# Kernel tuning notes

Hardware: AMD Instinct MI355X
Metric: run time of the kernel (lower is better)

## Reference

```python
import jax, jax.numpy as jnp
import numpy as np

INPUT_DIM = 1024
HIDDEN_DIM = 1024

def setup_inputs() -> dict:
    key = jax.random.key(0)
    ks = jax.random.split(key, 9)
    s_in = 1.0 / np.sqrt(INPUT_DIM)
    s_h = 1.0 / np.sqrt(HIDDEN_DIM)
    x = jax.random.normal(ks[0], (4, 2048, INPUT_DIM), dtype=jnp.float32)
    Wq = jax.random.uniform(ks[1], (INPUT_DIM, HIDDEN_DIM), jnp.float32, -s_in, s_in)
    bq = jax.random.uniform(ks[2], (HIDDEN_DIM,), jnp.float32, -s_in, s_in)
    Wk = jax.random.uniform(ks[3], (INPUT_DIM, HIDDEN_DIM), jnp.float32, -s_in, s_in)
    bk = jax.random.uniform(ks[4], (HIDDEN_DIM,), jnp.float32, -s_in, s_in)
    Wv = jax.random.uniform(ks[5], (INPUT_DIM, HIDDEN_DIM), jnp.float32, -s_in, s_in)
    bv = jax.random.uniform(ks[6], (HIDDEN_DIM,), jnp.float32, -s_in, s_in)
    Wo = jax.random.uniform(ks[7], (HIDDEN_DIM, INPUT_DIM), jnp.float32, -s_h, s_h)
    bo = jax.random.uniform(ks[8], (INPUT_DIM,), jnp.float32, -s_h, s_h)
    return {"x": x, "Wq": Wq, "bq": bq, "Wk": Wk, "bk": bk, "Wv": Wv, "bv": bv, "Wo": Wo, "bo": bo}

def reference(x, Wq, bq, Wk, bk, Wv, bv, Wo, bo):
    # x: [B, S, D_in]; scale uses x.shape[-1] (faithful to source, which divides by sqrt(input_dim))
    scale = 1.0 / jnp.sqrt(jnp.asarray(x.shape[-1], dtype=x.dtype))
    Q = jnp.einsum('bsd,dh->bsh', x, Wq) + bq
    K = jnp.einsum('bsd,dh->bsh', x, Wk) + bk
    V = jnp.einsum('bsd,dh->bsh', x, Wv) + bv
    scores = jnp.einsum('bqh,bkh->bqk', Q, K) * scale  # [B, S, S]
    attn = jax.nn.softmax(scores, axis=-1)
    ctx = jnp.einsum('bqk,bkh->bqh', attn, V)
    return jnp.einsum('bsh,hd->bsd', ctx, Wo) + bo
```

## Files before the change

### kernel.cpp

```cpp
#include <hip/hip_runtime.h>
#include <hip/hip_bf16.h>

typedef __attribute__((ext_vector_type(8))) short bf16x8;
typedef __attribute__((ext_vector_type(16))) float f32x16;

#define AS1 __attribute__((address_space(1)))
#define AS3 __attribute__((address_space(3)))

__device__ __forceinline__ unsigned short f2bf(float f) {
  unsigned u = __float_as_uint(f);
  u += 0x7fff + ((u >> 16) & 1);
  return (unsigned short)(u >> 16);
}

__device__ __forceinline__ void gload_lds16(const void* g, void* l) {
  __builtin_amdgcn_global_load_lds((const AS1 unsigned int*)g,
                                   (AS3 unsigned int*)l, 16, 0, 0);
}

template <typename OutT, bool BIAS, bool SPLIT>
__global__ __launch_bounds__(256) void gemm_bt(
    const unsigned short* __restrict__ A,
    const unsigned short* __restrict__ Bt,
    OutT* __restrict__ C,
    const float* __restrict__ bias,
    int Kd, int lda, int ldb, int ldc,
    long sA, long sB, long sC,
    float scale) {
  __shared__ unsigned short ldsA[128 * 32];
  __shared__ unsigned short ldsB[128 * 32];
  const int bz = blockIdx.z;
  A  += (size_t)bz * sA + (size_t)blockIdx.x * 128 * lda;
  Bt += (size_t)bz * sB + (size_t)blockIdx.y * 128 * ldb;

  const int tid  = threadIdx.x;
  const int wave = tid >> 6;
  const int lane = tid & 63;
  const int wm   = (wave >> 1) * 64;
  const int wn   = (wave & 1) * 64;
  const int l32  = lane & 31;
  const int half = lane >> 5;
  const int srow = wave * 16 + (lane >> 2);
  const int cg   = ((lane & 3) ^ ((lane >> 2) & 3) ^ (lane >> 4)) * 8;
  const int pswz = (l32 & 3) ^ ((l32 >> 2) & 3);

  f32x16 acc[2][2] = {};

  for (int k0 = 0; k0 < Kd; k0 += 32) {
    __syncthreads();
    gload_lds16(A  + (size_t)srow * lda + k0 + cg,        (char*)ldsA + wave * 1024);
    gload_lds16(A  + (size_t)(srow + 64) * lda + k0 + cg, (char*)ldsA + 4096 + wave * 1024);
    gload_lds16(Bt + (size_t)srow * ldb + k0 + cg,        (char*)ldsB + wave * 1024);
    gload_lds16(Bt + (size_t)(srow + 64) * ldb + k0 + cg, (char*)ldsB + 4096 + wave * 1024);
    __syncthreads();

    bf16x8 af[2][2], bfr[2][2];
#pragma unroll
    for (int t = 0; t < 2; ++t)
#pragma unroll
      for (int h = 0; h < 2; ++h) {
        const int p = ((2 * h + half) ^ pswz) * 8;
        af[t][h]  = *(const bf16x8*)&ldsA[(wm + t * 32 + l32) * 32 + p];
        bfr[t][h] = *(const bf16x8*)&ldsB[(wn + t * 32 + l32) * 32 + p];
      }
#pragma unroll
    for (int t = 0; t < 2; ++t)
#pragma unroll
      for (int u = 0; u < 2; ++u) {
        acc[t][u] = __builtin_amdgcn_mfma_f32_32x32x16_bf16(af[t][0], bfr[u][0], acc[t][u], 0, 0, 0);
        acc[t][u] = __builtin_amdgcn_mfma_f32_32x32x16_bf16(af[t][1], bfr[u][1], acc[t][u], 0, 0, 0);
      }
  }

  const int row0 = blockIdx.x * 128 + wm;
  const int col0glob = blockIdx.y * 128 + wn;
  int col0;
  if constexpr (SPLIT) {
    C += (size_t)((blockIdx.y * 128) >> 10) * sC;
    col0 = ((blockIdx.y * 128) & 1023) + wn;
  } else {
    C += (size_t)bz * sC;
    col0 = col0glob;
  }
#pragma unroll
  for (int t = 0; t < 2; ++t) {
#pragma unroll
    for (int u = 0; u < 2; ++u) {
      const int col = col0 + u * 32 + l32;
      const float bv = BIAS ? bias[col0glob + u * 32 + l32] : 0.0f;
#pragma unroll
      for (int r = 0; r < 16; ++r) {
        const int row = row0 + t * 32 + (r & 3) + 8 * (r >> 2) + 4 * half;
        const float v = acc[t][u][r] * scale + bv;
        if constexpr (sizeof(OutT) == 4)
          C[(size_t)row * ldc + col] = v;
        else
          C[(size_t)row * ldc + col] = (OutT)f2bf(v);
      }
    }
  }
}

__global__ void cvt_x(const float* __restrict__ in, unsigned short* __restrict__ out, int n4) {
  const int i = blockIdx.x * blockDim.x + threadIdx.x;
  if (i < n4) {
    const float4 v = ((const float4*)in)[i];
    uint2 o;
    o.x = (unsigned)f2bf(v.x) | ((unsigned)f2bf(v.y) << 16);
    o.y = (unsigned)f2bf(v.z) | ((unsigned)f2bf(v.w) << 16);
    ((uint2*)out)[i] = o;
  }
}

__global__ void cvtT_w4(const float* __restrict__ Wq, const float* __restrict__ Wk,
                        const float* __restrict__ Wv, const float* __restrict__ Wo,
                        unsigned short* __restrict__ Wqkvb, unsigned short* __restrict__ Wob) {
  __shared__ unsigned short tile[64][65];
  const int z = blockIdx.z;
  const float* in = (z == 0) ? Wq : (z == 1) ? Wk : (z == 2) ? Wv : Wo;
  unsigned short* out = (z == 3) ? Wob : Wqkvb + (size_t)z * 1024 * 1024;
  const int r0 = blockIdx.y * 64, c0 = blockIdx.x * 64;
  for (int i = threadIdx.y; i < 64; i += 4)
    tile[i][threadIdx.x] = f2bf(in[(size_t)(r0 + i) * 1024 + c0 + threadIdx.x]);
  __syncthreads();
  for (int i = threadIdx.y; i < 64; i += 4)
    out[(size_t)(c0 + i) * 1024 + r0 + threadIdx.x] = tile[threadIdx.x][i];
}

__global__ void concat_bias(const float* __restrict__ bq, const float* __restrict__ bk,
                            const float* __restrict__ bv, float* __restrict__ dst) {
  const int z = blockIdx.x;
  const float* src = (z == 0) ? bq : (z == 1) ? bk : bv;
  const int i = threadIdx.x;
  ((float4*)(dst + z * 1024))[i] = ((const float4*)src)[i];
}

__global__ void transpose_bf16(const unsigned short* __restrict__ in,
                               unsigned short* __restrict__ out, int rows, int cols) {
  __shared__ unsigned short tile[64][65];
  const int b = blockIdx.z;
  in  += (size_t)b * rows * cols;
  out += (size_t)b * rows * cols;
  const int r0 = blockIdx.y * 64, c0 = blockIdx.x * 64;
  for (int i = threadIdx.y; i < 64; i += 4)
    tile[i][threadIdx.x] = in[(size_t)(r0 + i) * cols + c0 + threadIdx.x];
  __syncthreads();
  for (int i = threadIdx.y; i < 64; i += 4)
    out[(size_t)(c0 + i) * rows + r0 + threadIdx.x] = tile[threadIdx.x][i];
}

__global__ __launch_bounds__(256) void softmax_inplace(float* __restrict__ scores) {
  float* p = scores + (size_t)blockIdx.x * 2048;
  const int t = threadIdx.x;
  float4 v0 = ((const float4*)p)[t * 2];
  float4 v1 = ((const float4*)p)[t * 2 + 1];

  float m = fmaxf(fmaxf(fmaxf(v0.x, v0.y), fmaxf(v0.z, v0.w)),
                  fmaxf(fmaxf(v1.x, v1.y), fmaxf(v1.z, v1.w)));
#pragma unroll
  for (int off = 32; off; off >>= 1) m = fmaxf(m, __shfl_xor(m, off, 64));

  __shared__ float red[4];
  __shared__ float bcast[2];
  const int wave = t >> 6, lane = t & 63;
  if (lane == 0) red[wave] = m;
  __syncthreads();
  if (t == 0) bcast[0] = fmaxf(fmaxf(red[0], red[1]), fmaxf(red[2], red[3]));
  __syncthreads();
  m = bcast[0];

  v0.x = __expf(v0.x - m); v0.y = __expf(v0.y - m);
  v0.z = __expf(v0.z - m); v0.w = __expf(v0.w - m);
  v1.x = __expf(v1.x - m); v1.y = __expf(v1.y - m);
  v1.z = __expf(v1.z - m); v1.w = __expf(v1.w - m);

  float s = v0.x + v0.y + v0.z + v0.w + v1.x + v1.y + v1.z + v1.w;
#pragma unroll
  for (int off = 32; off; off >>= 1) s += __shfl_xor(s, off, 64);
  if (lane == 0) red[wave] = s;
  __syncthreads();
  if (t == 0) bcast[1] = red[0] + red[1] + red[2] + red[3];
  __syncthreads();
  const float inv = 1.0f / bcast[1];

  uint4 ov;
  ov.x = (unsigned)f2bf(v0.x * inv) | ((unsigned)f2bf(v0.y * inv) << 16);
  ov.y = (unsigned)f2bf(v0.z * inv) | ((unsigned)f2bf(v0.w * inv) << 16);
  ov.z = (unsigned)f2bf(v1.x * inv) | ((unsigned)f2bf(v1.y * inv) << 16);
  ov.w = (unsigned)f2bf(v1.z * inv) | ((unsigned)f2bf(v1.w * inv) << 16);
  ((uint4*)p)[t] = ov;
}

extern "C" void kernel_launch(void* const* d_in, const int* in_sizes, int n_in,
                              void* d_out, int out_size, void* d_ws, size_t ws_size,
                              hipStream_t stream) {
  const float* x  = (const float*)d_in[0];
  const float* Wq = (const float*)d_in[1];
  const float* bq = (const float*)d_in[2];
  const float* Wk = (const float*)d_in[3];
  const float* bk = (const float*)d_in[4];
  const float* Wv = (const float*)d_in[5];
  const float* bv = (const float*)d_in[6];
  const float* Wo = (const float*)d_in[7];
  const float* bo = (const float*)d_in[8];
  float* out = (float*)d_out;

  char* ws = (char*)d_ws;
  size_t off = 0;
  auto alloc = [&](size_t bytes) { char* p = ws + off; off += (bytes + 255) & ~255UL; return p; };
  unsigned short* xb    = (unsigned short*)alloc(8192UL * 1024 * 2);
  unsigned short* Wqkvb = (unsigned short*)alloc(3072UL * 1024 * 2);
  unsigned short* Wob   = (unsigned short*)alloc(1024UL * 1024 * 2);
  float*          bqkv  = (float*)alloc(3072UL * 4);
  unsigned short* Qb    = (unsigned short*)alloc(8192UL * 1024 * 2);
  unsigned short* Kb    = (unsigned short*)alloc(8192UL * 1024 * 2);
  unsigned short* Vb    = (unsigned short*)alloc(8192UL * 1024 * 2);
  unsigned short* Vtb   = (unsigned short*)alloc(4UL * 1024 * 2048 * 2);
  unsigned short* ctxb  = (unsigned short*)alloc(8192UL * 1024 * 2);
  float*          sc    = (float*)alloc(4UL * 2048 * 2048 * 4);

  const dim3 blk(256);

  cvt_x<<<2097152 / 256, 256, 0, stream>>>(x, xb, 2097152);
  cvtT_w4<<<dim3(16, 16, 4), dim3(64, 4), 0, stream>>>(Wq, Wk, Wv, Wo, Wqkvb, Wob);
  concat_bias<<<3, 256, 0, stream>>>(bq, bk, bv, bqkv);

  gemm_bt<unsigned short, true, true><<<dim3(64, 24, 1), blk, 0, stream>>>(
      xb, Wqkvb, Qb, bqkv, 1024, 1024, 1024, 1024, 0, 0, 8192L * 1024, 1.0f);

  transpose_bf16<<<dim3(16, 32, 4), dim3(64, 4), 0, stream>>>(Vb, Vtb, 2048, 1024);

  gemm_bt<float, false, false><<<dim3(16, 16, 4), blk, 0, stream>>>(
      Qb, Kb, sc, nullptr, 1024, 1024, 1024, 2048,
      2048L * 1024, 2048L * 1024, 2048L * 2048, 0.03125f);

  softmax_inplace<<<8192, 256, 0, stream>>>(sc);

  gemm_bt<unsigned short, false, false><<<dim3(16, 8, 4), blk, 0, stream>>>(
      (unsigned short*)sc, Vtb, ctxb, nullptr, 2048, 4096, 2048, 1024,
      2048L * 4096, 1024L * 2048, 2048L * 1024, 1.0f);

  gemm_bt<float, true, false><<<dim3(64, 8, 1), blk, 0, stream>>>(
      ctxb, Wob, out, bo, 1024, 1024, 1024, 1024, 0, 0, 0, 1.0f);
}
```

Baseline: 328.5 us.

## Double-buffer GEMM LDS staging and widen N tile for large GEMMs

The bf16 MFMA GEMM now issues global-to-LDS loads for the next K slice into a second LDS buffer before computing on the current one, dropping one barrier per iteration. A template parameter NJ also widens the block's N tile to 256 for the QKV projection and QK^T GEMMs, so each A tile is reused across more columns, with launch grids halved to match. Launch bounds are tightened to hint occupancy. In exchange, more LDS and accumulator registers are used per block, which may lower occupancy. With only one barrier per iteration, correctness depends on the asynchronous global_load_lds writes into the other buffer not racing with reads from the previous iteration.

```diff
diff --git a/kernel.cpp b/kernel.cpp
--- a/kernel.cpp
+++ b/kernel.cpp
@@ -18,8 +18,8 @@
                                    (AS3 unsigned int*)l, 16, 0, 0);
 }
 
-template <typename OutT, bool BIAS, bool SPLIT>
-__global__ __launch_bounds__(256) void gemm_bt(
+template <typename OutT, bool BIAS, bool SPLIT, int NJ>
+__global__ __launch_bounds__(256, (NJ == 4) ? 2 : 3) void gemm_bt(
     const unsigned short* __restrict__ A,
     const unsigned short* __restrict__ Bt,
     OutT* __restrict__ C,
@@ -27,67 +27,86 @@
     int Kd, int lda, int ldb, int ldc,
     long sA, long sB, long sC,
     float scale) {
-  __shared__ unsigned short ldsA[128 * 32];
-  __shared__ unsigned short ldsB[128 * 32];
+  constexpr int BN    = NJ * 64;
+  constexpr int ROWS  = 128 + BN;
+  constexpr int SLOTS = ROWS / 16;
+  __shared__ unsigned short lds[2][ROWS * 32];
+
   const int bz = blockIdx.z;
   A  += (size_t)bz * sA + (size_t)blockIdx.x * 128 * lda;
-  Bt += (size_t)bz * sB + (size_t)blockIdx.y * 128 * ldb;
+  Bt += (size_t)bz * sB + (size_t)blockIdx.y * BN * ldb;
 
   const int tid  = threadIdx.x;
   const int wave = tid >> 6;
   const int lane = tid & 63;
   const int wm   = (wave >> 1) * 64;
-  const int wn   = (wave & 1) * 64;
+  const int wn   = (wave & 1) * (NJ * 32);
   const int l32  = lane & 31;
   const int half = lane >> 5;
-  const int srow = wave * 16 + (lane >> 2);
   const int cg   = ((lane & 3) ^ ((lane >> 2) & 3) ^ (lane >> 4)) * 8;
   const int pswz = (l32 & 3) ^ ((l32 >> 2) & 3);
 
-  f32x16 acc[2][2] = {};
-
+  auto stage = [&](int k0, int b) {
+#pragma unroll
+    for (int j = 0; j < SLOTS / 4; ++j) {
+      const int s = wave + 4 * j;
+      const int r = s * 16 + (lane >> 2);
+      const unsigned short* src = (s < 8) ? (A + (size_t)r * lda)
+                                          : (Bt + (size_t)(r - 128) * ldb);
+      gload_lds16(src + k0 + cg, (char*)&lds[b][0] + s * 1024);
+    }
+  };
+
+  f32x16 acc[2][NJ] = {};
+
+  stage(0, 0);
+  int cur = 0;
   for (int k0 = 0; k0 < Kd; k0 += 32) {
     __syncthreads();
-    gload_lds16(A  + (size_t)srow * lda + k0 + cg,        (char*)ldsA + wave * 1024);
-    gload_lds16(A  + (size_t)(srow + 64) * lda + k0 + cg, (char*)ldsA + 4096 + wave * 1024);
-    gload_lds16(Bt + (size_t)srow * ldb + k0 + cg,        (char*)ldsB + wave * 1024);
-    gload_lds16(Bt + (size_t)(srow + 64) * ldb + k0 + cg, (char*)ldsB + 4096 + wave * 1024);
-    __syncthreads();
-
-    bf16x8 af[2][2], bfr[2][2];
+    if (k0 + 32 < Kd) stage(k0 + 32, cur ^ 1);
+
+    const unsigned short* base = &lds[cur][0];
+    bf16x8 af[2][2], bfr[NJ][2];
 #pragma unroll
     for (int t = 0; t < 2; ++t)
 #pragma unroll
       for (int h = 0; h < 2; ++h) {
         const int p = ((2 * h + half) ^ pswz) * 8;
-        af[t][h]  = *(const bf16x8*)&ldsA[(wm + t * 32 + l32) * 32 + p];
-        bfr[t][h] = *(const bf16x8*)&ldsB[(wn + t * 32 + l32) * 32 + p];
+        af[t][h] = *(const bf16x8*)&base[(wm + t * 32 + l32) * 32 + p];
+      }
+#pragma unroll
+    for (int u = 0; u < NJ; ++u)
+#pragma unroll
+      for (int h = 0; h < 2; ++h) {
+        const int p = ((2 * h + half) ^ pswz) * 8;
+        bfr[u][h] = *(const bf16x8*)&base[(128 + wn + u * 32 + l32) * 32 + p];
       }
 #pragma unroll
     for (int t = 0; t < 2; ++t)
 #pragma unroll
-      for (int u = 0; u < 2; ++u) {
+      for (int u = 0; u < NJ; ++u) {
         acc[t][u] = __builtin_amdgcn_mfma_f32_32x32x16_bf16(af[t][0], bfr[u][0], acc[t][u], 0, 0, 0);
         acc[t][u] = __builtin_amdgcn_mfma_f32_32x32x16_bf16(af[t][1], bfr[u][1], acc[t][u], 0, 0, 0);
       }
+    cur ^= 1;
   }
 
   const int row0 = blockIdx.x * 128 + wm;
-  const int col0glob = blockIdx.y * 128 + wn;
+  const int colb = blockIdx.y * BN;
   int col0;
   if constexpr (SPLIT) {
-    C += (size_t)((blockIdx.y * 128) >> 10) * sC;
-    col0 = ((blockIdx.y * 128) & 1023) + wn;
+    C += (size_t)(colb >> 10) * sC;
+    col0 = (colb & 1023) + wn;
   } else {
     C += (size_t)bz * sC;
-    col0 = col0glob;
+    col0 = colb + wn;
   }
 #pragma unroll
   for (int t = 0; t < 2; ++t) {
 #pragma unroll
-    for (int u = 0; u < 2; ++u) {
+    for (int u = 0; u < NJ; ++u) {
       const int col = col0 + u * 32 + l32;
-      const float bv = BIAS ? bias[col0glob + u * 32 + l32] : 0.0f;
+      const float bv = BIAS ? bias[colb + wn + u * 32 + l32] : 0.0f;
 #pragma unroll
       for (int r = 0; r < 16; ++r) {
         const int row = row0 + t * 32 + (r & 3) + 8 * (r >> 2) + 4 * half;
@@ -225,21 +244,21 @@
   cvtT_w4<<<dim3(16, 16, 4), dim3(64, 4), 0, stream>>>(Wq, Wk, Wv, Wo, Wqkvb, Wob);
   concat_bias<<<3, 256, 0, stream>>>(bq, bk, bv, bqkv);
 
-  gemm_bt<unsigned short, true, true><<<dim3(64, 24, 1), blk, 0, stream>>>(
+  gemm_bt<unsigned short, true, true, 4><<<dim3(64, 12, 1), blk, 0, stream>>>(
       xb, Wqkvb, Qb, bqkv, 1024, 1024, 1024, 1024, 0, 0, 8192L * 1024, 1.0f);
 
   transpose_bf16<<<dim3(16, 32, 4), dim3(64, 4), 0, stream>>>(Vb, Vtb, 2048, 1024);
 
-  gemm_bt<float, false, false><<<dim3(16, 16, 4), blk, 0, stream>>>(
+  gemm_bt<float, false, false, 4><<<dim3(16, 8, 4), blk, 0, stream>>>(
       Qb, Kb, sc, nullptr, 1024, 1024, 1024, 2048,
       2048L * 1024, 2048L * 1024, 2048L * 2048, 0.03125f);
 
   softmax_inplace<<<8192, 256, 0, stream>>>(sc);
 
-  gemm_bt<unsigned short, false, false><<<dim3(16, 8, 4), blk, 0, stream>>>(
+  gemm_bt<unsigned short, false, false, 2><<<dim3(16, 8, 4), blk, 0, stream>>>(
       (unsigned short*)sc, Vtb, ctxb, nullptr, 2048, 4096, 2048, 1024,
       2048L * 4096, 1024L * 2048, 2048L * 1024, 1.0f);
 
-  gemm_bt<float, true, false><<<dim3(64, 8, 1), blk, 0, stream>>>(
+  gemm_bt<float, true, false, 2><<<dim3(64, 8, 1), blk, 0, stream>>>(
       ctxb, Wob, out, bo, 1024, 1024, 1024, 1024, 0, 0, 0, 1.0f);
 }
```

After: 317.6 us. -3.3%, faster.
